# Optimization experiments

Measured on AMD Instinct MI355X. Metric: run time of the kernel, lower is better.

## Reference

```python
import jax, jax.numpy as jnp
import numpy as np

B, D, H, L, T = 4096, 256, 512, 2, 45


def _lstm_cell(x, h, c, W_ih, W_hh, b_ih, b_hh):
    # PyTorch LSTM gate order: i, f, g, o
    gates = x @ W_ih + h @ W_hh + b_ih + b_hh  # [B, 4H]
    i, f, g, o = jnp.split(gates, 4, axis=-1)
    i = jax.nn.sigmoid(i)
    f = jax.nn.sigmoid(f)
    g = jnp.tanh(g)
    o = jax.nn.sigmoid(o)
    c_new = f * c + i * g
    h_new = o * jnp.tanh(c_new)
    return h_new, c_new


def setup_inputs() -> dict:
    key = jax.random.key(0)
    ks = jax.random.split(key, 32)
    s = 0.02
    inp = {
        "encoder_feat": jax.random.normal(ks[0], (B, D), jnp.float32),
        "context": jax.random.normal(ks[1], (B, D), jnp.float32),
        "initial_intent": jax.random.uniform(ks[2], (B, 1), jnp.float32),
        # hidden/cell init linears: d_model -> H*L (stored [in, out])
        "Wh_init": jax.random.normal(ks[3], (D, H * L), jnp.float32) * s,
        "bh_init": jnp.zeros((H * L,), jnp.float32),
        "Wc_init": jax.random.normal(ks[4], (D, H * L), jnp.float32) * s,
        "bc_init": jnp.zeros((H * L,), jnp.float32),
        # LSTM layer 0: input size 1 + d_model
        "W_ih0": jax.random.normal(ks[5], (1 + D, 4 * H), jnp.float32) * s,
        "W_hh0": jax.random.normal(ks[6], (H, 4 * H), jnp.float32) * s,
        "b_ih0": jnp.zeros((4 * H,), jnp.float32),
        "b_hh0": jnp.zeros((4 * H,), jnp.float32),
        # LSTM layer 1: input size H
        "W_ih1": jax.random.normal(ks[7], (H, 4 * H), jnp.float32) * s,
        "W_hh1": jax.random.normal(ks[8], (H, 4 * H), jnp.float32) * s,
        "b_ih1": jnp.zeros((4 * H,), jnp.float32),
        "b_hh1": jnp.zeros((4 * H,), jnp.float32),
        # output_proj: H -> 32 -> 1
        "Wo1": jax.random.normal(ks[9], (H, 32), jnp.float32) * s,
        "bo1": jnp.zeros((32,), jnp.float32),
        "Wo2": jax.random.normal(ks[10], (32, 1), jnp.float32) * s,
        "bo2": jnp.zeros((1,), jnp.float32),
        # global_intent_head: H -> 32 -> 1
        "Wg1": jax.random.normal(ks[11], (H, 32), jnp.float32) * s,
        "bg1": jnp.zeros((32,), jnp.float32),
        "Wg2": jax.random.normal(ks[12], (32, 1), jnp.float32) * s,
        "bg2": jnp.zeros((1,), jnp.float32),
    }
    return inp


def reference(encoder_feat, context, initial_intent,
              Wh_init, bh_init, Wc_init, bc_init,
              W_ih0, W_hh0, b_ih0, b_hh0,
              W_ih1, W_hh1, b_ih1, b_hh1,
              Wo1, bo1, Wo2, bo2, Wg1, bg1, Wg2, bg2):
    # init hidden/cell: [B, L*H] -> [B, L, H]; layer-major slices
    h_init = (encoder_feat @ Wh_init + bh_init).reshape(B, L, H)
    c_init = (encoder_feat @ Wc_init + bc_init).reshape(B, L, H)
    h0, h1 = h_init[:, 0], h_init[:, 1]
    c0, c1 = c_init[:, 0], c_init[:, 1]

    def step(carry, _):
        h0, c0, h1, c1, intent = carry
        x = jnp.concatenate([intent, context], axis=-1)  # [B, 1+D]
        h0n, c0n = _lstm_cell(x, h0, c0, W_ih0, W_hh0, b_ih0, b_hh0)
        h1n, c1n = _lstm_cell(h0n, h1, c1, W_ih1, W_hh1, b_ih1, b_hh1)
        logit = jax.nn.relu(h1n @ Wo1 + bo1) @ Wo2 + bo2  # [B, 1]
        intent_new = jax.nn.sigmoid(logit)
        return (h0n, c0n, h1n, c1n, intent_new), intent_new

    carry0 = (h0, c0, h1, c1, initial_intent)
    (h0, c0, h1, c1, _), ys = jax.lax.scan(step, carry0, None, length=T)
    step_intents = jnp.transpose(ys, (1, 0, 2))  # [B, T, 1]
    global_logit = jax.nn.relu(h1 @ Wg1 + bg1) @ Wg2 + bg2
    global_intent = jax.nn.sigmoid(global_logit)  # [B, 1]
    return step_intents, global_intent
```

## Files before the change

### kernel.cpp

```cpp
#include <hip/hip_runtime.h>
#include <hip/hip_bf16.h>

#define Bsz 4096
#define Dsz 256
#define Hsz 512
#define Tsz 45

typedef __attribute__((ext_vector_type(8))) short short8;
typedef __attribute__((ext_vector_type(4))) float f32x4;
typedef __attribute__((ext_vector_type(4))) unsigned short us4;
typedef __attribute__((ext_vector_type(2))) long lx2;
using bf16 = __hip_bfloat16;
using u8 = unsigned char;

__device__ __forceinline__ float sigf(float x)   { return 1.0f / (1.0f + __expf(-x)); }
__device__ __forceinline__ float tanhft(float x) { return 1.0f - 2.0f / (__expf(2.0f * x) + 1.0f); }
__device__ __forceinline__ float b2f(unsigned short u) { return __uint_as_float((unsigned)u << 16); }
__device__ __forceinline__ u8 f2fp8(float v) {
    int p = __builtin_amdgcn_cvt_pk_fp8_f32(v, v, 0, false);
    return (u8)(p & 0xff);
}

__device__ __forceinline__ void gload16(const void* g, void* l) {
    __builtin_amdgcn_global_load_lds((const __attribute__((address_space(1))) void*)g,
                                     (__attribute__((address_space(3))) void*)l, 16, 0, 0);
}

#define WAIT_VM(N) asm volatile("s_waitcnt vmcnt(" #N ")" ::: "memory")

__global__ void k_conv(const float* __restrict__ ef,   const float* __restrict__ ctx,
                       const float* __restrict__ Whi,  const float* __restrict__ Wci,
                       const float* __restrict__ Wih0, const float* __restrict__ Whh0,
                       const float* __restrict__ Wih1, const float* __restrict__ Whh1,
                       const float* __restrict__ Wo1,  const float* __restrict__ Wg1,
                       bf16* __restrict__ efb,  bf16* __restrict__ ctxb,
                       bf16* __restrict__ Wit,  u8* __restrict__ W0p,
                       u8* __restrict__ W1p,  u8* __restrict__ Wo1p,
                       u8* __restrict__ Wg1p)
{
    size_t tid = (size_t)blockIdx.x * blockDim.x + threadIdx.x;
    size_t gsz = (size_t)gridDim.x * blockDim.x;
    for (size_t i = tid; i < (size_t)Bsz * Dsz; i += gsz) {
        efb[i]  = __float2bfloat16(ef[i]);
        ctxb[i] = __float2bfloat16(ctx[i]);
    }
    for (size_t i = tid; i < 2048ull * 512 / 4; i += gsz) {
        int n = i >> 7, k = (i & 127) * 4;
        int lo = __builtin_amdgcn_cvt_pk_fp8_f32(Whh0[(size_t)(k+0)*2048+n], Whh0[(size_t)(k+1)*2048+n], 0, false);
        int pk = __builtin_amdgcn_cvt_pk_fp8_f32(Whh0[(size_t)(k+2)*2048+n], Whh0[(size_t)(k+3)*2048+n], lo, true);
        int nb = n >> 4;
        int q = ((nb >> 5) << 2) + (nb & 3);
        size_t dst = (((size_t)(k >> 5) * 8 + ((nb >> 2) & 7)) * 8 + (q >> 1)) * 1024
                   + ((k >> 3) & 3) * 256 + (n & 15) * 16 + (q & 1) * 8 + (k & 4);
        *(int*)(W0p + dst) = pk;
    }
    for (size_t i = tid; i < 2048ull * 1024 / 4; i += gsz) {
        int n = i >> 8, k = (i & 255) * 4;
        float f0, f1, f2, f3;
        if (k < 512) {
            f0 = Wih1[(size_t)(k+0)*2048+n]; f1 = Wih1[(size_t)(k+1)*2048+n];
            f2 = Wih1[(size_t)(k+2)*2048+n]; f3 = Wih1[(size_t)(k+3)*2048+n];
        } else {
            int kk = k - 512;
            f0 = Whh1[(size_t)(kk+0)*2048+n]; f1 = Whh1[(size_t)(kk+1)*2048+n];
            f2 = Whh1[(size_t)(kk+2)*2048+n]; f3 = Whh1[(size_t)(kk+3)*2048+n];
        }
        int lo = __builtin_amdgcn_cvt_pk_fp8_f32(f0, f1, 0, false);
        int pk = __builtin_amdgcn_cvt_pk_fp8_f32(f2, f3, lo, true);
        int nb = n >> 4;
        int q = ((nb >> 5) << 2) + (nb & 3);
        size_t dst = (((size_t)(k >> 5) * 8 + ((nb >> 2) & 7)) * 8 + (q >> 1)) * 1024
                   + ((k >> 3) & 3) * 256 + (n & 15) * 16 + (q & 1) * 8 + (k & 4);
        *(int*)(W1p + dst) = pk;
    }
    for (size_t i = tid; i < 32ull * 512 / 4; i += gsz) {
        int n = i >> 7, k = (i & 127) * 4;
        size_t dst = ((size_t)(n >> 4) * 16 + (k >> 5)) * 512 + ((k >> 3) & 3) * 128 + (n & 15) * 8 + (k & 4);
        int lo = __builtin_amdgcn_cvt_pk_fp8_f32(Wo1[(size_t)(k+0)*32+n], Wo1[(size_t)(k+1)*32+n], 0, false);
        int pk = __builtin_amdgcn_cvt_pk_fp8_f32(Wo1[(size_t)(k+2)*32+n], Wo1[(size_t)(k+3)*32+n], lo, true);
        *(int*)(Wo1p + dst) = pk;
        lo = __builtin_amdgcn_cvt_pk_fp8_f32(Wg1[(size_t)(k+0)*32+n], Wg1[(size_t)(k+1)*32+n], 0, false);
        pk = __builtin_amdgcn_cvt_pk_fp8_f32(Wg1[(size_t)(k+2)*32+n], Wg1[(size_t)(k+3)*32+n], lo, true);
        *(int*)(Wg1p + dst) = pk;
    }
    for (size_t i = tid; i < 4096ull * 256; i += gsz) {
        size_t n = i >> 8, k = i & 255;
        float v = (n < 1024) ? Whi[k * 1024 + n]
                : (n < 2048) ? Wci[k * 1024 + (n - 1024)]
                             : Wih0[(1 + k) * 2048 + (n - 2048)];
        Wit[i] = __float2bfloat16(v);
    }
}

__global__ void __launch_bounds__(256)
k_init(const bf16* __restrict__ efb, const bf16* __restrict__ ctxb,
       const bf16* __restrict__ Wit,
       const float* __restrict__ bh,  const float* __restrict__ bc,
       const float* __restrict__ bi0, const float* __restrict__ bh0,
       u8* __restrict__ h0, u8* __restrict__ h1,
       float* __restrict__ c0, float* __restrict__ c1,
       bf16* __restrict__ ctxg)
{
    const int t = threadIdx.x, lane = t & 63, w = t >> 6;
    const int wr = w >> 1, wc = w & 1;
    const int lq = lane >> 4, ln = lane & 15;
    const int m0 = blockIdx.x * 128, n0 = blockIdx.y * 64;
    const bf16* A = (n0 < 2048) ? efb : ctxb;

    f32x4 zero = {0.f, 0.f, 0.f, 0.f};
    f32x4 acc[4][2];
#pragma unroll
    for (int r = 0; r < 4; ++r)
#pragma unroll
        for (int c = 0; c < 2; ++c) acc[r][c] = zero;

    for (int k0 = 0; k0 < 256; k0 += 32) {
        short8 af[4];
#pragma unroll
        for (int r = 0; r < 4; ++r)
            af[r] = *(const short8*)(A + (size_t)(m0 + wr * 64 + r * 16 + ln) * 256 + k0 + lq * 8);
#pragma unroll
        for (int c = 0; c < 2; ++c) {
            short8 bv = *(const short8*)(Wit + (size_t)(n0 + wc * 32 + c * 16 + ln) * 256 + k0 + lq * 8);
#pragma unroll
            for (int r = 0; r < 4; ++r)
                acc[r][c] = __builtin_amdgcn_mfma_f32_16x16x32_bf16(af[r], bv, acc[r][c], 0, 0, 0);
        }
    }
#pragma unroll
    for (int r = 0; r < 4; ++r)
#pragma unroll
        for (int c = 0; c < 2; ++c)
#pragma unroll
            for (int e = 0; e < 4; ++e) {
                int b = m0 + wr * 64 + r * 16 + lq * 4 + e;
                int n = n0 + wc * 32 + c * 16 + ln;
                float v = acc[r][c][e];
                if (n < 1024) {
                    v += bh[n];
                    if (n < 512) h0[(size_t)b * 512 + n]       = f2fp8(v);
                    else         h1[(size_t)b * 512 + n - 512] = f2fp8(v);
                } else if (n < 2048) {
                    int m = n - 1024; v += bc[m];
                    if (m < 512) c0[(size_t)b * 512 + m]       = v;
                    else         c1[(size_t)b * 512 + m - 512] = v;
                } else {
                    int j = n - 2048;
                    ctxg[(size_t)b * 2048 + (j & 511) * 4 + (j >> 9)] =
                        __float2bfloat16(v + bi0[j] + bh0[j]);
                }
            }
}

__device__ __forceinline__ long hread(const u8* buf, int ln, int lq, int kt) {
    int c = (kt << 2) + lq;
    return *(const long*)(buf + ln * 512 + ((c ^ ln) << 3));
}

__device__ __forceinline__ void stageH(const u8* __restrict__ Wp, int w, int h,
                                       u8* Wr, int lane) {
    const u8* src = Wp + ((size_t)((h >> 1) * 8 + w) << 13) + ((size_t)(h & 1) << 12) + lane * 16;
    u8* dst = Wr + ((size_t)(h & 3) << 12);
#pragma unroll
    for (int i = 0; i < 4; ++i)
        gload16(src + i * 1024, dst + i * 1024);
}

template <int QB>
__device__ __forceinline__ void mfma_half(const u8* slot, int lane, long bf,
                                          f32x4 (&acc)[4][4]) {
#pragma unroll
    for (int i = 0; i < 4; ++i) {
        lx2 v = *(const lx2*)(slot + i * 1024 + lane * 16);
        acc[(QB + 2 * i) & 3][(QB + 2 * i) >> 2] =
            __builtin_amdgcn_mfma_f32_16x16x32_fp8_fp8(v[0], bf, acc[(QB + 2 * i) & 3][(QB + 2 * i) >> 2], 0, 0, 0);
        acc[(QB + 2 * i + 1) & 3][(QB + 2 * i + 1) >> 2] =
            __builtin_amdgcn_mfma_f32_16x16x32_fp8_fp8(v[1], bf, acc[(QB + 2 * i + 1) & 3][(QB + 2 * i + 1) >> 2], 0, 0, 0);
    }
}

__global__ void __launch_bounds__(512, 1)
k_loop(const u8* __restrict__ h0i, const u8* __restrict__ h1i,
       const u8* __restrict__ W0p, const u8* __restrict__ W1p,
       const u8* __restrict__ Wo1p, const u8* __restrict__ Wg1p,
       const bf16* __restrict__ ctxg, const float* __restrict__ ii,
       const float* __restrict__ w0row,
       const float* __restrict__ bi1, const float* __restrict__ bh1,
       const float* __restrict__ bo1, const float* __restrict__ Wo2,
       const float* __restrict__ bo2,
       const float* __restrict__ bg1, const float* __restrict__ Wg2,
       const float* __restrict__ bg2,
       const float* __restrict__ c0g, const float* __restrict__ c1g,
       float* __restrict__ out)
{
    __shared__ u8 h0L[8192];
    __shared__ u8 h1L[8192];
    __shared__ u8 WringS[8][16384];
    __shared__ unsigned short a0Lb[2048];
    __shared__ unsigned short a1Lb[2048];
    __shared__ float sit[16];
    __shared__ float spart[16][2];

    const int t = threadIdx.x, lane = t & 63, w = t >> 6;
    const int ln = lane & 15, lq = lane >> 4;
    const int m0 = blockIdx.x * 16;
    const int b = m0 + ln;
    u8* Wr = WringS[w];
    f32x4 zero = {0.f, 0.f, 0.f, 0.f};

#pragma unroll
    for (int i = 0; i < 2; ++i) {
        int cid = i * 512 + t;
        int row = cid >> 6, c = cid & 63;
        long v0 = *(const long*)(h0i + (size_t)(m0 + row) * 512 + c * 8);
        long v1 = *(const long*)(h1i + (size_t)(m0 + row) * 512 + c * 8);
        int pc = row * 512 + ((c ^ row) << 3);
        *(long*)(&h0L[pc]) = v0;
        *(long*)(&h1L[pc]) = v1;
    }
#pragma unroll
    for (int i = 0; i < 4; ++i) {
        int idx = i * 512 + t;
        a0Lb[idx] = (unsigned short)(__bfloat16_as_ushort(__float2bfloat16(w0row[idx])));
        a1Lb[idx] = (unsigned short)(__bfloat16_as_ushort(__float2bfloat16(bi1[idx] + bh1[idx])));
    }
    f32x4 cr0[4], cr1[4];
    us4 xg[4][4];
#pragma unroll
    for (int jc = 0; jc < 4; ++jc) {
        int jlb = (w * 4 + jc) * 16 + lq * 4;
        cr0[jc] = *(const f32x4*)(c0g + (size_t)b * 512 + jlb);
        cr1[jc] = *(const f32x4*)(c1g + (size_t)b * 512 + jlb);
#pragma unroll
        for (int e = 0; e < 4; ++e)
            xg[jc][e] = *(const us4*)((const unsigned short*)ctxg + (size_t)b * 2048 + (jlb + e) * 4);
    }
    __syncthreads();

    auto head2 = [&](const u8* Wp, const float* b1, const float* W2, float b2s,
                     bool tosit, float* dst, int stride, int scol) {
        if (w < 2) {
            f32x4 acc = zero;
#pragma unroll
            for (int kt = 0; kt < 16; ++kt) {
                long bf = hread(h1L, ln, lq, kt);
                long af = *(const long*)(Wp + (size_t)(w * 16 + kt) * 512 + lane * 8);
                acc = __builtin_amdgcn_mfma_f32_16x16x32_fp8_fp8(af, bf, acc, 0, 0, 0);
            }
            float v = 0.f;
#pragma unroll
            for (int e = 0; e < 4; ++e) {
                int j = w * 16 + lq * 4 + e;
                v += fmaxf(acc[e] + b1[j], 0.f) * W2[j];
            }
            v += __shfl_xor(v, 16);
            v += __shfl_xor(v, 32);
            if (lq == 0) spart[ln][w] = v;
        }
        __syncthreads();
        if (t < 16) {
            float pv = sigf(spart[t][0] + spart[t][1] + b2s);
            if (tosit) sit[t] = pv;
            if (dst) dst[(size_t)(m0 + t) * stride + scol] = pv;
        }
        __syncthreads();
    };

    stageH(W0p, w, 0, Wr, lane);
    stageH(W0p, w, 1, Wr, lane);
    stageH(W0p, w, 2, Wr, lane);

    for (int s = 0; s < Tsz; ++s) {
        if (s == 0) {
            if (t < 16) sit[t] = ii[m0 + t];
            __syncthreads();
        } else {
            head2(Wo1p, bo1, Wo2, bo2[0], true, out, Tsz, s - 1);
        }
        const float sval = sit[ln];

        {
            f32x4 acc[4][4];
#pragma unroll
            for (int jc = 0; jc < 4; ++jc)
#pragma unroll
                for (int g = 0; g < 4; ++g) acc[jc][g] = zero;

#pragma unroll 2
            for (int kt = 0; kt < 14; ++kt) {
                long bf = hread(h0L, ln, lq, kt);
                WAIT_VM(8);
                mfma_half<0>(Wr + (size_t)((2 * kt) & 3) * 4096, lane, bf, acc);
                stageH(W0p, w, 2 * kt + 3, Wr, lane);
                WAIT_VM(8);
                mfma_half<8>(Wr + (size_t)((2 * kt + 1) & 3) * 4096, lane, bf, acc);
                stageH(W0p, w, 2 * kt + 4, Wr, lane);
            }
            {
                long bf = hread(h0L, ln, lq, 14);
                WAIT_VM(8);
                mfma_half<0>(Wr + (size_t)(28 & 3) * 4096, lane, bf, acc);
                stageH(W0p, w, 31, Wr, lane);
                WAIT_VM(8);
                mfma_half<8>(Wr + (size_t)(29 & 3) * 4096, lane, bf, acc);
                stageH(W1p, w, 0, Wr, lane);
            }
            {
                long bf = hread(h0L, ln, lq, 15);
                WAIT_VM(8);
                mfma_half<0>(Wr + (size_t)(30 & 3) * 4096, lane, bf, acc);
                stageH(W1p, w, 1, Wr, lane);
                WAIT_VM(8);
                mfma_half<8>(Wr + (size_t)(31 & 3) * 4096, lane, bf, acc);
                stageH(W1p, w, 2, Wr, lane);
            }
            int hold[4];
#pragma unroll
            for (int jc = 0; jc < 4; ++jc) {
                int jlb = (w * 4 + jc) * 16 + lq * 4;
                us4 a0v[4];
#pragma unroll
                for (int g = 0; g < 4; ++g) a0v[g] = *(const us4*)(a0Lb + g * 512 + jlb);
                float hv[4];
#pragma unroll
                for (int e = 0; e < 4; ++e) {
                    float pre[4];
#pragma unroll
                    for (int g = 0; g < 4; ++g)
                        pre[g] = acc[jc][g][e] + b2f(xg[jc][e][g]) + sval * b2f(a0v[g][e]);
                    float ig = sigf(pre[0]), fg = sigf(pre[1]);
                    float gg = tanhft(pre[2]), og = sigf(pre[3]);
                    float cn = fg * cr0[jc][e] + ig * gg;
                    cr0[jc][e] = cn;
                    hv[e] = og * tanhft(cn);
                }
                int lo = __builtin_amdgcn_cvt_pk_fp8_f32(hv[0], hv[1], 0, false);
                hold[jc] = __builtin_amdgcn_cvt_pk_fp8_f32(hv[2], hv[3], lo, true);
            }
            __syncthreads();
#pragma unroll
            for (int jc = 0; jc < 4; ++jc) {
                int c = (w * 4 + jc) * 2 + (lq >> 1);
                *(int*)(h0L + ln * 512 + ((c ^ ln) << 3) + (lq & 1) * 4) = hold[jc];
            }
            asm volatile("s_waitcnt lgkmcnt(0)" ::: "memory");
            __syncthreads();
        }

        {
            f32x4 acc[4][4];
#pragma unroll
            for (int jc = 0; jc < 4; ++jc)
#pragma unroll
                for (int g = 0; g < 4; ++g) acc[jc][g] = zero;

#pragma unroll 2
            for (int kt = 0; kt < 16; ++kt) {
                long bf = hread(h0L, ln, lq, kt);
                WAIT_VM(8);
                mfma_half<0>(Wr + (size_t)((2 * kt) & 3) * 4096, lane, bf, acc);
                stageH(W1p, w, 2 * kt + 3, Wr, lane);
                WAIT_VM(8);
                mfma_half<8>(Wr + (size_t)((2 * kt + 1) & 3) * 4096, lane, bf, acc);
                stageH(W1p, w, 2 * kt + 4, Wr, lane);
            }
#pragma unroll 2
            for (int kt = 16; kt < 30; ++kt) {
                long bf = hread(h1L, ln, lq, kt - 16);
                WAIT_VM(8);
                mfma_half<0>(Wr + (size_t)((2 * kt) & 3) * 4096, lane, bf, acc);
                stageH(W1p, w, 2 * kt + 3, Wr, lane);
                WAIT_VM(8);
                mfma_half<8>(Wr + (size_t)((2 * kt + 1) & 3) * 4096, lane, bf, acc);
                stageH(W1p, w, 2 * kt + 4, Wr, lane);
            }
            {
                long bf = hread(h1L, ln, lq, 14);
                WAIT_VM(8);
                mfma_half<0>(Wr + (size_t)(60 & 3) * 4096, lane, bf, acc);
                stageH(W1p, w, 63, Wr, lane);
                WAIT_VM(8);
                mfma_half<8>(Wr + (size_t)(61 & 3) * 4096, lane, bf, acc);
                stageH(W0p, w, 0, Wr, lane);
            }
            {
                long bf = hread(h1L, ln, lq, 15);
                WAIT_VM(8);
                mfma_half<0>(Wr + (size_t)(62 & 3) * 4096, lane, bf, acc);
                stageH(W0p, w, 1, Wr, lane);
                WAIT_VM(8);
                mfma_half<8>(Wr + (size_t)(63 & 3) * 4096, lane, bf, acc);
                stageH(W0p, w, 2, Wr, lane);
            }
            int hold[4];
#pragma unroll
            for (int jc = 0; jc < 4; ++jc) {
                int jlb = (w * 4 + jc) * 16 + lq * 4;
                us4 a1v[4];
#pragma unroll
                for (int g = 0; g < 4; ++g) a1v[g] = *(const us4*)(a1Lb + g * 512 + jlb);
                float hv[4];
#pragma unroll
                for (int e = 0; e < 4; ++e) {
                    float pre[4];
#pragma unroll
                    for (int g = 0; g < 4; ++g) pre[g] = acc[jc][g][e] + b2f(a1v[g][e]);
                    float ig = sigf(pre[0]), fg = sigf(pre[1]);
                    float gg = tanhft(pre[2]), og = sigf(pre[3]);
                    float cn = fg * cr1[jc][e] + ig * gg;
                    cr1[jc][e] = cn;
                    hv[e] = og * tanhft(cn);
                }
                int lo = __builtin_amdgcn_cvt_pk_fp8_f32(hv[0], hv[1], 0, false);
                hold[jc] = __builtin_amdgcn_cvt_pk_fp8_f32(hv[2], hv[3], lo, true);
            }
            __syncthreads();
#pragma unroll
            for (int jc = 0; jc < 4; ++jc) {
                int c = (w * 4 + jc) * 2 + (lq >> 1);
                *(int*)(h1L + ln * 512 + ((c ^ ln) << 3) + (lq & 1) * 4) = hold[jc];
            }
            asm volatile("s_waitcnt lgkmcnt(0)" ::: "memory");
            __syncthreads();
        }
    }

    head2(Wo1p, bo1, Wo2, bo2[0], false, out, Tsz, 44);
    head2(Wg1p, bg1, Wg2, bg2[0], false, out + (size_t)Bsz * Tsz, 1, 0);
}

extern "C" void kernel_launch(void* const* d_in, const int* in_sizes, int n_in,
                              void* d_out, int out_size, void* d_ws, size_t ws_size,
                              hipStream_t stream)
{
    const float* ef   = (const float*)d_in[0];
    const float* ctx  = (const float*)d_in[1];
    const float* ii   = (const float*)d_in[2];
    const float* Whi  = (const float*)d_in[3];
    const float* bh   = (const float*)d_in[4];
    const float* Wci  = (const float*)d_in[5];
    const float* bc   = (const float*)d_in[6];
    const float* Wih0 = (const float*)d_in[7];
    const float* Whh0 = (const float*)d_in[8];
    const float* bi0  = (const float*)d_in[9];
    const float* bh0  = (const float*)d_in[10];
    const float* Wih1 = (const float*)d_in[11];
    const float* Whh1 = (const float*)d_in[12];
    const float* bi1  = (const float*)d_in[13];
    const float* bh1  = (const float*)d_in[14];
    const float* Wo1  = (const float*)d_in[15];
    const float* bo1  = (const float*)d_in[16];
    const float* Wo2  = (const float*)d_in[17];
    const float* bo2  = (const float*)d_in[18];
    const float* Wg1  = (const float*)d_in[19];
    const float* bg1  = (const float*)d_in[20];
    const float* Wg2  = (const float*)d_in[21];
    const float* bg2  = (const float*)d_in[22];
    float* out = (float*)d_out;

    char* ws = (char*)d_ws;
    size_t off = 0;
    auto take = [&](size_t bytes) -> char* {
        char* pp = ws + off;
        off += (bytes + 255) & ~(size_t)255;
        return pp;
    };
    u8*  W0p     = (u8*)take(2048ull * 512);
    u8*  W1p     = (u8*)take(2048ull * 1024);
    u8*  Wo1p    = (u8*)take(32ull * 512);
    u8*  Wg1p    = (u8*)take(32ull * 512);
    bf16* Wit    = (bf16*)take(4096ull * 256 * 2);
    bf16* efb    = (bf16*)take((size_t)Bsz * Dsz * 2);
    bf16* ctxb   = (bf16*)take((size_t)Bsz * Dsz * 2);
    u8*  h0x     = (u8*)take((size_t)Bsz * Hsz);
    u8*  h1x     = (u8*)take((size_t)Bsz * Hsz);
    float* c0    = (float*)take((size_t)Bsz * Hsz * 4);
    float* c1    = (float*)take((size_t)Bsz * Hsz * 4);
    bf16* ctxg   = (bf16*)take((size_t)Bsz * 2048 * 2);
    (void)ws_size; (void)in_sizes; (void)n_in; (void)out_size;

    k_conv<<<2048, 256, 0, stream>>>(ef, ctx, Whi, Wci, Wih0, Whh0, Wih1, Whh1, Wo1, Wg1,
                                     efb, ctxb, Wit, W0p, W1p, Wo1p, Wg1p);
    k_init<<<dim3(32, 64), 256, 0, stream>>>(efb, ctxb, Wit, bh, bc, bi0, bh0,
                                             h0x, h1x, c0, c1, ctxg);
    k_loop<<<256, 512, 0, stream>>>(h0x, h1x, W0p, W1p, Wo1p, Wg1p,
                                    ctxg, ii, Wih0, bi1, bh1,
                                    bo1, Wo2, bo2, bg1, Wg2, bg2,
                                    c0, c1, out);
}
```

Baseline: 2.405 ms.

## Stream weight tiles into registers instead of an LDS ring via global_load_lds

Weight tiles for the recurrent matmuls are now loaded straight from global memory into a four-deep rotating set of register buffers, replacing the per-wave 16 KB LDS ring filled by global_load_lds. This removes the LDS round trip (the async write plus the ds_read before each MFMA) and frees 128 KB of shared memory. The cost is more VGPR pressure from 16 lx2 buffers on top of the accumulators. The vmcnt-based wait accounting now depends on register-destination loads, and the compiler may reorder or serialize them, which could weaken the prefetch overlap.

After: 3.648 ms. 51.7% more time.

```diff
diff --git a/kernel.cpp b/kernel.cpp
--- a/kernel.cpp
+++ b/kernel.cpp
@@ -19,11 +19,6 @@
 __device__ __forceinline__ u8 f2fp8(float v) {
     int p = __builtin_amdgcn_cvt_pk_fp8_f32(v, v, 0, false);
     return (u8)(p & 0xff);
-}
-
-__device__ __forceinline__ void gload16(const void* g, void* l) {
-    __builtin_amdgcn_global_load_lds((const __attribute__((address_space(1))) void*)g,
-                                     (__attribute__((address_space(3))) void*)l, 16, 0, 0);
 }
 
 #define WAIT_VM(N) asm volatile("s_waitcnt vmcnt(" #N ")" ::: "memory")
@@ -157,25 +152,22 @@
     return *(const long*)(buf + ln * 512 + ((c ^ ln) << 3));
 }
 
-__device__ __forceinline__ void stageH(const u8* __restrict__ Wp, int w, int h,
-                                       u8* Wr, int lane) {
+__device__ __forceinline__ void loadH(const u8* __restrict__ Wp, int w, int h,
+                                      lx2 (&buf)[4], int lane) {
     const u8* src = Wp + ((size_t)((h >> 1) * 8 + w) << 13) + ((size_t)(h & 1) << 12) + lane * 16;
-    u8* dst = Wr + ((size_t)(h & 3) << 12);
 #pragma unroll
     for (int i = 0; i < 4; ++i)
-        gload16(src + i * 1024, dst + i * 1024);
+        buf[i] = *(const lx2*)(src + i * 1024);
 }
 
 template <int QB>
-__device__ __forceinline__ void mfma_half(const u8* slot, int lane, long bf,
-                                          f32x4 (&acc)[4][4]) {
+__device__ __forceinline__ void mfma8(const lx2 (&buf)[4], long bf, f32x4 (&acc)[4][4]) {
 #pragma unroll
     for (int i = 0; i < 4; ++i) {
-        lx2 v = *(const lx2*)(slot + i * 1024 + lane * 16);
         acc[(QB + 2 * i) & 3][(QB + 2 * i) >> 2] =
-            __builtin_amdgcn_mfma_f32_16x16x32_fp8_fp8(v[0], bf, acc[(QB + 2 * i) & 3][(QB + 2 * i) >> 2], 0, 0, 0);
+            __builtin_amdgcn_mfma_f32_16x16x32_fp8_fp8(buf[i][0], bf, acc[(QB + 2 * i) & 3][(QB + 2 * i) >> 2], 0, 0, 0);
         acc[(QB + 2 * i + 1) & 3][(QB + 2 * i + 1) >> 2] =
-            __builtin_amdgcn_mfma_f32_16x16x32_fp8_fp8(v[1], bf, acc[(QB + 2 * i + 1) & 3][(QB + 2 * i + 1) >> 2], 0, 0, 0);
+            __builtin_amdgcn_mfma_f32_16x16x32_fp8_fp8(buf[i][1], bf, acc[(QB + 2 * i + 1) & 3][(QB + 2 * i + 1) >> 2], 0, 0, 0);
     }
 }
 
@@ -195,7 +187,6 @@
 {
     __shared__ u8 h0L[8192];
     __shared__ u8 h1L[8192];
-    __shared__ u8 WringS[8][16384];
     __shared__ unsigned short a0Lb[2048];
     __shared__ unsigned short a1Lb[2048];
     __shared__ float sit[16];
@@ -205,7 +196,6 @@
     const int ln = lane & 15, lq = lane >> 4;
     const int m0 = blockIdx.x * 16;
     const int b = m0 + ln;
-    u8* Wr = WringS[w];
     f32x4 zero = {0.f, 0.f, 0.f, 0.f};
 
 #pragma unroll
@@ -266,9 +256,11 @@
         __syncthreads();
     };
 
-    stageH(W0p, w, 0, Wr, lane);
-    stageH(W0p, w, 1, Wr, lane);
-    stageH(W0p, w, 2, Wr, lane);
+    lx2 wf0[4], wf1[4], wf2[4], wf3[4];
+
+    loadH(W0p, w, 0, wf0, lane);
+    loadH(W0p, w, 1, wf1, lane);
+    loadH(W0p, w, 2, wf2, lane);
 
     for (int s = 0; s < Tsz; ++s) {
         if (s == 0) {
@@ -286,33 +278,21 @@
 #pragma unroll
                 for (int g = 0; g < 4; ++g) acc[jc][g] = zero;
 
-#pragma unroll 2
-            for (int kt = 0; kt < 14; ++kt) {
-                long bf = hread(h0L, ln, lq, kt);
-                WAIT_VM(8);
-                mfma_half<0>(Wr + (size_t)((2 * kt) & 3) * 4096, lane, bf, acc);
-                stageH(W0p, w, 2 * kt + 3, Wr, lane);
-                WAIT_VM(8);
-                mfma_half<8>(Wr + (size_t)((2 * kt + 1) & 3) * 4096, lane, bf, acc);
-                stageH(W0p, w, 2 * kt + 4, Wr, lane);
+            for (int k2 = 0; k2 < 7; ++k2) {
+                long bfa = hread(h0L, ln, lq, 2 * k2);
+                WAIT_VM(8); mfma8<0>(wf0, bfa, acc); loadH(W0p, w, 4 * k2 + 3, wf3, lane);
+                WAIT_VM(8); mfma8<8>(wf1, bfa, acc); loadH(W0p, w, 4 * k2 + 4, wf0, lane);
+                long bfb = hread(h0L, ln, lq, 2 * k2 + 1);
+                WAIT_VM(8); mfma8<0>(wf2, bfb, acc); loadH(W0p, w, 4 * k2 + 5, wf1, lane);
+                WAIT_VM(8); mfma8<8>(wf3, bfb, acc); loadH(W0p, w, 4 * k2 + 6, wf2, lane);
             }
             {
-                long bf = hread(h0L, ln, lq, 14);
-                WAIT_VM(8);
-                mfma_half<0>(Wr + (size_t)(28 & 3) * 4096, lane, bf, acc);
-                stageH(W0p, w, 31, Wr, lane);
-                WAIT_VM(8);
-                mfma_half<8>(Wr + (size_t)(29 & 3) * 4096, lane, bf, acc);
-                stageH(W1p, w, 0, Wr, lane);
-            }
-            {
-                long bf = hread(h0L, ln, lq, 15);
-                WAIT_VM(8);
-                mfma_half<0>(Wr + (size_t)(30 & 3) * 4096, lane, bf, acc);
-                stageH(W1p, w, 1, Wr, lane);
-                WAIT_VM(8);
-                mfma_half<8>(Wr + (size_t)(31 & 3) * 4096, lane, bf, acc);
-                stageH(W1p, w, 2, Wr, lane);
+                long bfa = hread(h0L, ln, lq, 14);
+                WAIT_VM(8); mfma8<0>(wf0, bfa, acc); loadH(W0p, w, 31, wf3, lane);
+                WAIT_VM(8); mfma8<8>(wf1, bfa, acc); loadH(W1p, w, 0, wf0, lane);
+                long bfb = hread(h0L, ln, lq, 15);
+                WAIT_VM(8); mfma8<0>(wf2, bfb, acc); loadH(W1p, w, 1, wf1, lane);
+                WAIT_VM(8); mfma8<8>(wf3, bfb, acc); loadH(W1p, w, 2, wf2, lane);
             }
             int hold[4];
 #pragma unroll
@@ -354,43 +334,29 @@
 #pragma unroll
                 for (int g = 0; g < 4; ++g) acc[jc][g] = zero;
 
-#pragma unroll 2
-            for (int kt = 0; kt < 16; ++kt) {
-                long bf = hread(h0L, ln, lq, kt);
-                WAIT_VM(8);
-                mfma_half<0>(Wr + (size_t)((2 * kt) & 3) * 4096, lane, bf, acc);
-                stageH(W1p, w, 2 * kt + 3, Wr, lane);
-                WAIT_VM(8);
-                mfma_half<8>(Wr + (size_t)((2 * kt + 1) & 3) * 4096, lane, bf, acc);
-                stageH(W1p, w, 2 * kt + 4, Wr, lane);
-            }
-#pragma unroll 2
-            for (int kt = 16; kt < 30; ++kt) {
-                long bf = hread(h1L, ln, lq, kt - 16);
-                WAIT_VM(8);
-                mfma_half<0>(Wr + (size_t)((2 * kt) & 3) * 4096, lane, bf, acc);
-                stageH(W1p, w, 2 * kt + 3, Wr, lane);
-                WAIT_VM(8);
-                mfma_half<8>(Wr + (size_t)((2 * kt + 1) & 3) * 4096, lane, bf, acc);
-                stageH(W1p, w, 2 * kt + 4, Wr, lane);
+            for (int k2 = 0; k2 < 8; ++k2) {
+                long bfa = hread(h0L, ln, lq, 2 * k2);
+                WAIT_VM(8); mfma8<0>(wf0, bfa, acc); loadH(W1p, w, 4 * k2 + 3, wf3, lane);
+                WAIT_VM(8); mfma8<8>(wf1, bfa, acc); loadH(W1p, w, 4 * k2 + 4, wf0, lane);
+                long bfb = hread(h0L, ln, lq, 2 * k2 + 1);
+                WAIT_VM(8); mfma8<0>(wf2, bfb, acc); loadH(W1p, w, 4 * k2 + 5, wf1, lane);
+                WAIT_VM(8); mfma8<8>(wf3, bfb, acc); loadH(W1p, w, 4 * k2 + 6, wf2, lane);
+            }
+            for (int k2 = 8; k2 < 15; ++k2) {
+                long bfa = hread(h1L, ln, lq, 2 * k2 - 16);
+                WAIT_VM(8); mfma8<0>(wf0, bfa, acc); loadH(W1p, w, 4 * k2 + 3, wf3, lane);
+                WAIT_VM(8); mfma8<8>(wf1, bfa, acc); loadH(W1p, w, 4 * k2 + 4, wf0, lane);
+                long bfb = hread(h1L, ln, lq, 2 * k2 - 15);
+                WAIT_VM(8); mfma8<0>(wf2, bfb, acc); loadH(W1p, w, 4 * k2 + 5, wf1, lane);
+                WAIT_VM(8); mfma8<8>(wf3, bfb, acc); loadH(W1p, w, 4 * k2 + 6, wf2, lane);
             }
             {
-                long bf = hread(h1L, ln, lq, 14);
-                WAIT_VM(8);
-                mfma_half<0>(Wr + (size_t)(60 & 3) * 4096, lane, bf, acc);
-                stageH(W1p, w, 63, Wr, lane);
-                WAIT_VM(8);
-                mfma_half<8>(Wr + (size_t)(61 & 3) * 4096, lane, bf, acc);
-                stageH(W0p, w, 0, Wr, lane);
-            }
-            {
-                long bf = hread(h1L, ln, lq, 15);
-                WAIT_VM(8);
-                mfma_half<0>(Wr + (size_t)(62 & 3) * 4096, lane, bf, acc);
-                stageH(W0p, w, 1, Wr, lane);
-                WAIT_VM(8);
-                mfma_half<8>(Wr + (size_t)(63 & 3) * 4096, lane, bf, acc);
-                stageH(W0p, w, 2, Wr, lane);
+                long bfa = hread(h1L, ln, lq, 14);
+                WAIT_VM(8); mfma8<0>(wf0, bfa, acc); loadH(W1p, w, 63, wf3, lane);
+                WAIT_VM(8); mfma8<8>(wf1, bfa, acc); loadH(W0p, w, 0, wf0, lane);
+                long bfb = hread(h1L, ln, lq, 15);
+                WAIT_VM(8); mfma8<0>(wf2, bfb, acc); loadH(W0p, w, 1, wf1, lane);
+                WAIT_VM(8); mfma8<8>(wf3, bfb, acc); loadH(W0p, w, 2, wf2, lane);
             }
             int hold[4];
 #pragma unroll
```
